# Performance work log

Measured on AMD Instinct MI355X. Metric: run time of the kernel, lower is better.

## Reference

```python
import jax, jax.numpy as jnp
import numpy as np

D_MODEL = 1024
H = 16
D_K = D_MODEL // H
D_FF = 4096
EPS = 1e-6
NEG = -1e9


def layernorm(x, alpha, bias):
    # custom LN: unbiased std (ddof=1), scalar alpha/bias, divide by (std+eps)
    mean = jnp.mean(x, axis=-1, keepdims=True)
    n = x.shape[-1]
    var = jnp.sum((x - mean) ** 2, axis=-1, keepdims=True) / (n - 1)
    std = jnp.sqrt(var)
    return alpha * (x - mean) / (std + EPS) + bias


def setup_inputs() -> dict:
    key = jax.random.key(0)
    ks = jax.random.split(key, 16)
    B, S = 2, 2048
    s = 1.0 / np.sqrt(D_MODEL)
    inp = {
        "x": jax.random.normal(ks[0], (B, S, D_MODEL), jnp.float32),
        "src_mask": jnp.ones((B, 1, S), jnp.int32),
        "wq": jax.random.normal(ks[1], (D_MODEL, D_MODEL), jnp.float32) * s,
        "bq": jnp.zeros((D_MODEL,), jnp.float32),
        "wk": jax.random.normal(ks[2], (D_MODEL, D_MODEL), jnp.float32) * s,
        "bk": jnp.zeros((D_MODEL,), jnp.float32),
        "wv": jax.random.normal(ks[3], (D_MODEL, D_MODEL), jnp.float32) * s,
        "bv": jnp.zeros((D_MODEL,), jnp.float32),
        "wo": jax.random.normal(ks[4], (D_MODEL, D_MODEL), jnp.float32) * s,
        "bo": jnp.zeros((D_MODEL,), jnp.float32),
        "w1": jax.random.normal(ks[5], (D_MODEL, D_FF), jnp.float32) * s,
        "b1": jnp.zeros((D_FF,), jnp.float32),
        "w2": jax.random.normal(ks[6], (D_FF, D_MODEL), jnp.float32) * (1.0 / np.sqrt(D_FF)),
        "b2": jnp.zeros((D_MODEL,), jnp.float32),
        "ln1_a": jnp.ones((1,), jnp.float32),
        "ln1_b": jnp.zeros((1,), jnp.float32),
        "ln2_a": jnp.ones((1,), jnp.float32),
        "ln2_b": jnp.zeros((1,), jnp.float32),
    }
    return inp


def reference(x, src_mask, wq, bq, wk, bk, wv, bv, wo, bo,
              w1, b1, w2, b2, ln1_a, ln1_b, ln2_a, ln2_b):
    B, S, _ = x.shape
    # --- residual 1: pre-norm self attention ---
    xn = layernorm(x, ln1_a, ln1_b)
    q = (xn @ wq + bq).reshape(B, S, H, D_K)
    k = (xn @ wk + bk).reshape(B, S, H, D_K)
    v = (xn @ wv + bv).reshape(B, S, H, D_K)
    # scores [B, H, S, S]
    scores = jnp.einsum("bqhd,bkhd->bhqk", q, k) / jnp.sqrt(jnp.float32(D_K))
    m = src_mask[:, None, :, :]  # [B,1,1,S]
    scores = jnp.where(m == 0, NEG, scores)
    attn = jax.nn.softmax(scores, axis=-1)
    ctx = jnp.einsum("bhqk,bkhd->bqhd", attn, v).reshape(B, S, D_MODEL)
    attn_out = ctx @ wo + bo
    x = x + attn_out
    # --- residual 2: pre-norm FFN ---
    xn = layernorm(x, ln2_a, ln2_b)
    ff = jax.nn.relu(xn @ w1 + b1) @ w2 + b2
    return x + ff
```

## Files before the change

### kernel.cpp

```cpp
#include <hip/hip_runtime.h>
#include <hip/hip_bf16.h>

typedef __attribute__((ext_vector_type(8))) short short8;
typedef __attribute__((ext_vector_type(4))) float f32x4;
typedef __attribute__((ext_vector_type(4))) unsigned int u32x4;
using u16 = unsigned short;
typedef unsigned int u32;

__device__ __forceinline__ u16 f2bf(float f) {
    u32 u = __builtin_bit_cast(u32, f);
    u32 r = u + 0x7FFFu + ((u >> 16) & 1u);
    return (u16)(r >> 16);
}

__device__ __forceinline__ float exp2fast(float x) {
    return __builtin_amdgcn_exp2f(x);
}

__device__ __forceinline__ u32 cvtpk(float lo, float hi) {
    u32 r;
    asm("v_cvt_pk_bf16_f32 %0, %1, %2" : "=v"(r) : "v"(lo), "v"(hi));
    return r;
}

__device__ __forceinline__ void async_load16(const void* g, void* l) {
    __builtin_amdgcn_global_load_lds(
        (const __attribute__((address_space(1))) void*)g,
        (__attribute__((address_space(3))) void*)l, 16, 0, 0);
}

__device__ __forceinline__ void wg_barrier() {
    asm volatile("" ::: "memory");
    __builtin_amdgcn_s_barrier();
    asm volatile("" ::: "memory");
}

__global__ __launch_bounds__(256) void convt_kernel(const float* __restrict__ w,
                                                    u16* __restrict__ wt, int K, int N) {
    __shared__ float tile[32][33];
    int bn = blockIdx.x * 32, bk = blockIdx.y * 32;
    int tx = threadIdx.x & 31, ty = threadIdx.x >> 5;
#pragma unroll
    for (int i = 0; i < 4; i++)
        tile[ty + i * 8][tx] = w[(size_t)(bk + ty + i * 8) * N + bn + tx];
    __syncthreads();
#pragma unroll
    for (int i = 0; i < 4; i++)
        wt[(size_t)(bn + ty + i * 8) * K + bk + tx] = f2bf(tile[tx][ty + i * 8]);
}

__global__ __launch_bounds__(256) void convt4_kernel(const float* __restrict__ wa,
                                                     const float* __restrict__ wb,
                                                     const float* __restrict__ wc,
                                                     const float* __restrict__ wd,
                                                     u16* __restrict__ da,
                                                     u16* __restrict__ db,
                                                     u16* __restrict__ dc,
                                                     u16* __restrict__ dd) {
    __shared__ float tile[32][33];
    int z = blockIdx.z;
    const float* w = (z == 0) ? wa : (z == 1) ? wb : (z == 2) ? wc : wd;
    u16* wt = (z == 0) ? da : (z == 1) ? db : (z == 2) ? dc : dd;
    int bn = blockIdx.x * 32, bk = blockIdx.y * 32;
    int tx = threadIdx.x & 31, ty = threadIdx.x >> 5;
#pragma unroll
    for (int i = 0; i < 4; i++)
        tile[ty + i * 8][tx] = w[(size_t)(bk + ty + i * 8) * 1024 + bn + tx];
    __syncthreads();
#pragma unroll
    for (int i = 0; i < 4; i++)
        wt[(size_t)(bn + ty + i * 8) * 1024 + bk + tx] = f2bf(tile[tx][ty + i * 8]);
}

__global__ __launch_bounds__(256) void vtrans_kernel(const u16* __restrict__ qkv,
                                                     u16* __restrict__ vT) {
    __shared__ u16 tile[32][33];
    int bs = blockIdx.x * 32;
    int bc = blockIdx.y * 32;
    int b  = blockIdx.z;
    int tx = threadIdx.x & 31, ty = threadIdx.x >> 5;
#pragma unroll
    for (int i = 0; i < 4; i++)
        tile[ty + i * 8][tx] = qkv[(size_t)(b * 2048 + bs + ty + i * 8) * 3072 + 2048 + bc + tx];
    __syncthreads();
#pragma unroll
    for (int i = 0; i < 4; i++)
        vT[(size_t)(b * 1024 + bc + ty + i * 8) * 2048 + bs + tx] = tile[tx][ty + i * 8];
}

__global__ __launch_bounds__(256) void ln_kernel(const float* __restrict__ x,
                                                 const float* __restrict__ ga,
                                                 const float* __restrict__ gb,
                                                 u16* __restrict__ out) {
    int row = blockIdx.x;
    const float4* xr = (const float4*)(x + (size_t)row * 1024);
    float4 v = xr[threadIdx.x];
    float s  = v.x + v.y + v.z + v.w;
    float s2 = v.x * v.x + v.y * v.y + v.z * v.z + v.w * v.w;
#pragma unroll
    for (int off = 32; off; off >>= 1) {
        s  += __shfl_down(s, off);
        s2 += __shfl_down(s2, off);
    }
    __shared__ float rs[4], rs2[4];
    int wid = threadIdx.x >> 6, lane = threadIdx.x & 63;
    if (lane == 0) { rs[wid] = s; rs2[wid] = s2; }
    __syncthreads();
    float S  = rs[0] + rs[1] + rs[2] + rs[3];
    float S2 = rs2[0] + rs2[1] + rs2[2] + rs2[3];
    float mean = S * (1.0f / 1024.0f);
    float var  = fmaxf((S2 - 1024.0f * mean * mean) * (1.0f / 1023.0f), 0.0f);
    float scale = ga[0] / (sqrtf(var) + 1e-6f);
    float shift = gb[0] - mean * scale;
    u16 h0 = f2bf(v.x * scale + shift);
    u16 h1 = f2bf(v.y * scale + shift);
    u16 h2 = f2bf(v.z * scale + shift);
    u16 h3 = f2bf(v.w * scale + shift);
    uint2 pv;
    pv.x = (u32)h0 | ((u32)h1 << 16);
    pv.y = (u32)h2 | ((u32)h3 << 16);
    *(uint2*)(out + (size_t)row * 1024 + threadIdx.x * 4) = pv;
}

__global__ __launch_bounds__(256) void bias3_kernel(const float* __restrict__ a,
                                                    const float* __restrict__ b,
                                                    const float* __restrict__ c,
                                                    float* __restrict__ d) {
    int i = blockIdx.x * 256 + threadIdx.x;
    float v = (i < 1024) ? a[i] : ((i < 2048) ? b[i - 1024] : c[i - 2048]);
    d[i] = v;
}

__global__ __launch_bounds__(256) void addbias_kernel(float* __restrict__ dst,
                                                      const float* __restrict__ p,
                                                      const float* __restrict__ bias,
                                                      const float* __restrict__ resid) {
    int i4 = blockIdx.x * 256 + threadIdx.x;
    float4 d  = ((const float4*)dst)[i4];
    float4 pp = ((const float4*)p)[i4];
    float4 rr = ((const float4*)resid)[i4];
    float4 bb = *(const float4*)(bias + ((i4 * 4) & 1023));
    d.x += pp.x + bb.x + rr.x;
    d.y += pp.y + bb.y + rr.y;
    d.z += pp.z + bb.z + rr.z;
    d.w += pp.w + bb.w + rr.w;
    ((float4*)dst)[i4] = d;
}

template <int RELU>
__global__ __launch_bounds__(512) void gemm256_bt(const u16* __restrict__ A,
                                                  const u16* __restrict__ Bt,
                                                  const float* __restrict__ bias,
                                                  u16* __restrict__ C,
                                                  int M, int N, int K, int tilesN) {
    __shared__ u16 lds[2][2][16384];
    const int tid = threadIdx.x;
    const int lane = tid & 63, wid = tid >> 6;
    const int l15 = lane & 15, l4 = lane >> 4;
    const int wm = wid >> 2, wn = wid & 3;

    int nwg = gridDim.x;
    int bid = blockIdx.x;
    int swz = (bid & 7) * (nwg >> 3) + (bid >> 3);
    int ty = swz / tilesN, tx = swz % tilesN;

    const u16* Ag = A + (size_t)(ty * 256) * K;
    const u16* Bg = Bt + (size_t)(tx * 256) * K;

    auto stage_half = [&](int slot, int ab, int half, const u16* G, int k0) {
#pragma unroll
        for (int j = 0; j < 2; j++) {
            int off16 = half * 1024 + j * 512 + tid;
            int r = off16 >> 3;
            int gs = (off16 & 7) ^ (r & 7);
            const u16* src = G + (size_t)r * K + k0 + gs * 8;
            u16* dst = &lds[slot][ab][(size_t)(half * 1024 + j * 512 + (wid << 6)) * 8];
            async_load16(src, dst);
        }
    };

    f32x4 acc[8][4] = {};
    const int nT = K >> 6;

    stage_half(0, 0, 0, Ag, 0);
    stage_half(0, 0, 1, Ag, 0);
    stage_half(0, 1, 0, Bg, 0);
    stage_half(0, 1, 1, Bg, 0);
    __builtin_amdgcn_sched_barrier(0);

    for (int t = 0; t < nT; ++t) {
        const int cs = t & 1, ns = cs ^ 1;
        const int k1 = (t + 1) << 6;
        const bool pf = (t + 1 < nT);
#pragma unroll
        for (int ph = 0; ph < 4; ++ph) {
            if (ph == 0 && pf) { stage_half(ns, 0, 0, Ag, k1); stage_half(ns, 0, 1, Ag, k1); }
            if (ph == 1 && pf) { stage_half(ns, 1, 0, Bg, k1); stage_half(ns, 1, 1, Bg, k1); }
            __builtin_amdgcn_sched_barrier(0);
            if (ph == 0) {
                if (pf) asm volatile("s_waitcnt vmcnt(4)" ::: "memory");
                else    asm volatile("s_waitcnt vmcnt(0)" ::: "memory");
            }
            wg_barrier();

            const int rh = ph >> 1, ch = ph & 1;
            const u16* la = &lds[cs][0][0];
            const u16* lb = &lds[cs][1][0];
            short8 af[4][2], bf[2][2];
#pragma unroll
            for (int m2 = 0; m2 < 4; m2++) {
                int ra = wm * 128 + rh * 64 + m2 * 16 + l15;
#pragma unroll
                for (int ks = 0; ks < 2; ks++) {
                    int sl = (l4 + ks * 4) ^ (ra & 7);
                    af[m2][ks] = *(const short8*)&la[ra * 64 + sl * 8];
                }
            }
#pragma unroll
            for (int n2 = 0; n2 < 2; n2++) {
                int rb = wn * 64 + ch * 32 + n2 * 16 + l15;
#pragma unroll
                for (int ks = 0; ks < 2; ks++) {
                    int sl = (l4 + ks * 4) ^ (rb & 7);
                    bf[n2][ks] = *(const short8*)&lb[rb * 64 + sl * 8];
                }
            }
            __builtin_amdgcn_s_setprio(1);
#pragma unroll
            for (int m2 = 0; m2 < 4; m2++)
#pragma unroll
                for (int n2 = 0; n2 < 2; n2++)
#pragma unroll
                    for (int ks = 0; ks < 2; ks++)
                        acc[rh * 4 + m2][ch * 2 + n2] = __builtin_amdgcn_mfma_f32_16x16x32_bf16(
                            af[m2][ks], bf[n2][ks], acc[rh * 4 + m2][ch * 2 + n2], 0, 0, 0);
            __builtin_amdgcn_s_setprio(0);
            wg_barrier();
        }
    }

#pragma unroll
    for (int mi = 0; mi < 8; mi++) {
        int row0 = ty * 256 + wm * 128 + (mi >> 2) * 64 + (mi & 3) * 16 + l4 * 4;
#pragma unroll
        for (int ni = 0; ni < 4; ni++) {
            int col = tx * 256 + wn * 64 + (ni >> 1) * 32 + (ni & 1) * 16 + l15;
            float bc = bias[col];
#pragma unroll
            for (int jj = 0; jj < 4; jj++) {
                float v = acc[mi][ni][jj] + bc;
                if (RELU) v = fmaxf(v, 0.0f);
                C[(size_t)(row0 + jj) * N + col] = f2bf(v);
            }
        }
    }
}

template <int MODE, int RELU, int RESID>
__global__ __launch_bounds__(256) void gemm_bt(const u16* __restrict__ A,
                                               const u16* __restrict__ Bt,
                                               const float* __restrict__ bias,
                                               void* __restrict__ C0,
                                               void* __restrict__ C1,
                                               const float* __restrict__ resid,
                                               int M, int N, int K, int kLen) {
    __shared__ u16 As[8192];
    __shared__ u16 Bs[8192];
    int tid = threadIdx.x, lane = tid & 63, wid = tid >> 6;
    int l15 = lane & 15, l4 = lane >> 4;
    int rowA0 = blockIdx.x * 128;
    int rowB0 = blockIdx.y * 128;
    int kOff = blockIdx.z * kLen;
    void* Cout = blockIdx.z ? C1 : C0;
    int waveM = wid >> 1, waveN = wid & 1;

    int fl = tid * 8;
    int r0 = fl >> 5, c0 = fl & 31;
    const u16* gA0 = A + (size_t)(rowA0 + r0) * K + c0 + kOff;
    const u16* gA1 = A + (size_t)(rowA0 + 64 + r0) * K + c0 + kOff;
    const u16* gB0 = Bt + (size_t)(rowB0 + r0) * K + c0 + kOff;
    const u16* gB1 = Bt + (size_t)(rowB0 + 64 + r0) * K + c0 + kOff;

    f32x4 acc[4][4] = {};
    const int nIter = kLen >> 5;

    async_load16(gA0, As + wid * 512);
    async_load16(gA1, As + 2048 + wid * 512);
    async_load16(gB0, Bs + wid * 512);
    async_load16(gB1, Bs + 2048 + wid * 512);

    int cur = 0, kb = 32;
    for (int it = 0; it < nIter; ++it) {
        asm volatile("s_waitcnt vmcnt(0)" ::: "memory");
        __builtin_amdgcn_s_barrier();
        if (it + 1 < nIter) {
            u16* a = As + (cur ^ 1) * 4096;
            u16* bb = Bs + (cur ^ 1) * 4096;
            async_load16(gA0 + kb, a + wid * 512);
            async_load16(gA1 + kb, a + 2048 + wid * 512);
            async_load16(gB0 + kb, bb + wid * 512);
            async_load16(gB1 + kb, bb + 2048 + wid * 512);
        }
        __builtin_amdgcn_sched_barrier(0);

        const u16* a = As + cur * 4096;
        const u16* bb = Bs + cur * 4096;
        short8 af[4], bf[4];
#pragma unroll
        for (int m = 0; m < 4; m++)
            af[m] = *(const short8*)&a[(waveM * 64 + m * 16 + l15) * 32 + l4 * 8];
#pragma unroll
        for (int n = 0; n < 4; n++)
            bf[n] = *(const short8*)&bb[(waveN * 64 + n * 16 + l15) * 32 + l4 * 8];
#pragma unroll
        for (int m = 0; m < 4; m++)
#pragma unroll
            for (int n = 0; n < 4; n++)
                acc[m][n] = __builtin_amdgcn_mfma_f32_16x16x32_bf16(af[m], bf[n], acc[m][n], 0, 0, 0);

        __builtin_amdgcn_s_barrier();
        cur ^= 1;
        kb += 32;
    }

#pragma unroll
    for (int m = 0; m < 4; m++) {
        int row = rowA0 + waveM * 64 + m * 16 + l4 * 4;
#pragma unroll
        for (int n = 0; n < 4; n++) {
            int col = rowB0 + waveN * 64 + n * 16 + l15;
            float bc = (MODE == 2) ? 0.0f : bias[col];
#pragma unroll
            for (int j = 0; j < 4; j++) {
                float v = acc[m][n][j] + bc;
                if (RELU) v = fmaxf(v, 0.0f);
                if (RESID) v += resid[(size_t)(row + j) * N + col];
                if (MODE == 1)
                    ((u16*)Cout)[(size_t)(row + j) * N + col] = f2bf(v);
                else
                    ((float*)Cout)[(size_t)(row + j) * N + col] = v;
            }
        }
    }
}

__global__ __launch_bounds__(256) void attn_kernel(const u16* __restrict__ qkv,
                                                   const u16* __restrict__ vT,
                                                   const int* __restrict__ mask,
                                                   u16* __restrict__ ctx) {
    const int S = 2048;
    const float C = 0.180336880f;
    int qt = blockIdx.x;
    int bh = blockIdx.y;
    int b = bh >> 4, h = bh & 15;
    int tid = threadIdx.x;
    int wid = tid >> 6, lane = tid & 63;
    int l15 = lane & 15, l4 = lane >> 4;

    __shared__ u16 Ks[64][72];
    __shared__ u16 Vs[64][72];
    __shared__ int mflag;

    if (tid == 0) mflag = 1;
    __syncthreads();
    {
        const int* mrow = mask + b * S;
        int ok = 1;
#pragma unroll
        for (int i = 0; i < 8; i++) ok &= (mrow[tid * 8 + i] != 0);
        if (!ok) mflag = 0;
    }

    int qrow0 = qt * 64 + wid * 16;
    const u16* qb = qkv + (size_t)(b * S + qrow0) * 3072 + h * 64;
    short8 qf0 = *(const short8*)(qb + (size_t)l15 * 3072 + l4 * 8);
    short8 qf1 = *(const short8*)(qb + (size_t)l15 * 3072 + 32 + l4 * 8);

    f32x4 o[4] = {};
    float m_i = -1e30f, lp = 0.0f;
    __syncthreads();
    const int allones = mflag;
    const int* mrow = mask + b * S;

    int srow = tid >> 3, c8 = (tid & 7) * 8;
    short8 kreg[2], vreg[2];
#pragma unroll
    for (int p = 0; p < 2; p++) {
        int r = p * 32 + srow;
        kreg[p] = *(const short8*)(qkv + (size_t)(b * S + r) * 3072 + 1024 + h * 64 + c8);
        vreg[p] = *(const short8*)(vT + (size_t)(bh * 64 + r) * 2048 + c8);
    }

    for (int kt = 0; kt < 32; ++kt) {
        __builtin_amdgcn_s_barrier();
#pragma unroll
        for (int p = 0; p < 2; p++) {
            int r = p * 32 + srow;
            *(short8*)&Ks[r][c8] = kreg[p];
            *(short8*)&Vs[r][c8] = vreg[p];
        }
        if (kt + 1 < 32) {
#pragma unroll
            for (int p = 0; p < 2; p++) {
                int r = p * 32 + srow;
                kreg[p] = *(const short8*)(qkv + (size_t)(b * S + (kt + 1) * 64 + r) * 3072 + 1024 + h * 64 + c8);
                vreg[p] = *(const short8*)(vT + (size_t)(bh * 64 + r) * 2048 + (kt + 1) * 64 + c8);
            }
        }
        asm volatile("s_waitcnt lgkmcnt(0)" ::: "memory");
        __builtin_amdgcn_s_barrier();

        float sc[4][4];
#pragma unroll
        for (int kc = 0; kc < 4; kc++) {
            short8 kf0 = *(const short8*)&Ks[kc * 16 + l15][l4 * 8];
            short8 kf1 = *(const short8*)&Ks[kc * 16 + l15][32 + l4 * 8];
            f32x4 a = {};
            a = __builtin_amdgcn_mfma_f32_16x16x32_bf16(kf0, qf0, a, 0, 0, 0);
            a = __builtin_amdgcn_mfma_f32_16x16x32_bf16(kf1, qf1, a, 0, 0, 0);
            if (allones) {
#pragma unroll
                for (int j = 0; j < 4; j++) sc[kc][j] = a[j];
            } else {
#pragma unroll
                for (int j = 0; j < 4; j++) {
                    int mk = mrow[kt * 64 + kc * 16 + l4 * 4 + j];
                    sc[kc][j] = mk ? a[j] : -1e9f;
                }
            }
        }

        float lm = sc[0][0];
#pragma unroll
        for (int kc = 0; kc < 4; kc++)
#pragma unroll
            for (int j = 0; j < 4; j++) lm = fmaxf(lm, sc[kc][j]);
        if (!__all(lm <= m_i + 64.0f)) {
            float t = lm;
            t = fmaxf(t, __shfl_xor(t, 16));
            t = fmaxf(t, __shfl_xor(t, 32));
            float newm = fmaxf(m_i, t);
            float r = exp2fast((m_i - newm) * C);
            lp *= r;
            float rr0 = __shfl(r, l4 * 4 + 0);
            float rr1 = __shfl(r, l4 * 4 + 1);
            float rr2 = __shfl(r, l4 * 4 + 2);
            float rr3 = __shfl(r, l4 * 4 + 3);
#pragma unroll
            for (int dc = 0; dc < 4; dc++) {
                o[dc][0] *= rr0; o[dc][1] *= rr1; o[dc][2] *= rr2; o[dc][3] *= rr3;
            }
            m_i = newm;
        }

        float nb = -m_i * C;
        u32 pk[4][2];
#pragma unroll
        for (int kc = 0; kc < 4; kc++) {
            float p0 = exp2fast(fmaf(sc[kc][0], C, nb));
            float p1 = exp2fast(fmaf(sc[kc][1], C, nb));
            float p2 = exp2fast(fmaf(sc[kc][2], C, nb));
            float p3 = exp2fast(fmaf(sc[kc][3], C, nb));
            lp += (p0 + p1) + (p2 + p3);
            pk[kc][0] = cvtpk(p0, p1);
            pk[kc][1] = cvtpk(p2, p3);
        }

        u32 w0[4], w1[4];
#pragma unroll
        for (int i = 0; i < 4; i++) {
            int idx = l15 + (((2 * l4 + (i >> 1)) & 3) << 4);
            int tt = i & 1;
            u32 a0 = (u32)__shfl((int)pk[0][tt], idx);
            u32 a1 = (u32)__shfl((int)pk[1][tt], idx);
            u32 a2 = (u32)__shfl((int)pk[2][tt], idx);
            u32 a3 = (u32)__shfl((int)pk[3][tt], idx);
            w0[i] = (l4 < 2) ? a0 : a1;
            w1[i] = (l4 < 2) ? a2 : a3;
        }
        u32x4 v0 = {w0[0], w0[1], w0[2], w0[3]};
        u32x4 v1 = {w1[0], w1[1], w1[2], w1[3]};
        short8 pa0 = __builtin_bit_cast(short8, v0);
        short8 pa1 = __builtin_bit_cast(short8, v1);

#pragma unroll
        for (int dc = 0; dc < 4; dc++) {
            short8 vf0 = *(const short8*)&Vs[dc * 16 + l15][l4 * 8];
            short8 vf1 = *(const short8*)&Vs[dc * 16 + l15][32 + l4 * 8];
            o[dc] = __builtin_amdgcn_mfma_f32_16x16x32_bf16(pa0, vf0, o[dc], 0, 0, 0);
            o[dc] = __builtin_amdgcn_mfma_f32_16x16x32_bf16(pa1, vf1, o[dc], 0, 0, 0);
        }
    }

    float lt = lp;
    lt += __shfl_xor(lt, 16);
    lt += __shfl_xor(lt, 32);
    float inv = 1.0f / lt;
    float iv0 = __shfl(inv, l4 * 4 + 0);
    float iv1 = __shfl(inv, l4 * 4 + 1);
    float iv2 = __shfl(inv, l4 * 4 + 2);
    float iv3 = __shfl(inv, l4 * 4 + 3);
#pragma unroll
    for (int j = 0; j < 4; j++) {
        float ivj = (j == 0) ? iv0 : (j == 1) ? iv1 : (j == 2) ? iv2 : iv3;
        int row = qrow0 + l4 * 4 + j;
        size_t base = (size_t)(b * S + row) * 1024 + h * 64;
#pragma unroll
        for (int dc = 0; dc < 4; dc++)
            ctx[base + dc * 16 + l15] = f2bf(o[dc][j] * ivj);
    }
}

extern "C" void kernel_launch(void* const* d_in, const int* in_sizes, int n_in,
                              void* d_out, int out_size, void* d_ws, size_t ws_size,
                              hipStream_t stream) {
    const float* x    = (const float*)d_in[0];
    const int*   mask = (const int*)d_in[1];
    const float* wq   = (const float*)d_in[2];
    const float* bq   = (const float*)d_in[3];
    const float* wk   = (const float*)d_in[4];
    const float* bk   = (const float*)d_in[5];
    const float* wv   = (const float*)d_in[6];
    const float* bv   = (const float*)d_in[7];
    const float* wo   = (const float*)d_in[8];
    const float* bo   = (const float*)d_in[9];
    const float* w1   = (const float*)d_in[10];
    const float* b1   = (const float*)d_in[11];
    const float* w2   = (const float*)d_in[12];
    const float* b2   = (const float*)d_in[13];
    const float* ln1a = (const float*)d_in[14];
    const float* ln1b = (const float*)d_in[15];
    const float* ln2a = (const float*)d_in[16];
    const float* ln2b = (const float*)d_in[17];
    float* out = (float*)d_out;

    char* ws = (char*)d_ws;
    u16*   wqkvt = (u16*)(ws + 0);
    u16*   wot   = (u16*)(ws + 6291456);
    u16*   w1t   = (u16*)(ws + 8388608);
    u16*   w2t   = (u16*)(ws + 16777216);
    float* bqkv  = (float*)(ws + 25165824);
    char*  regA  = ws + 26214400;
    u16*   xn1   = (u16*)(regA + 0);
    u16*   vT    = (u16*)(regA + 0);
    u16*   qkv   = (u16*)(regA + 8388608);
    u16*   ctx   = (u16*)(regA + 33554432);
    float* p0wo  = (float*)(regA + 0);
    float* x1    = (float*)(ws + 68157440);
    u16*   xn2   = (u16*)(regA + 0);
    u16*   ff1   = (u16*)(regA + 8388608);
    float* p0f2  = (float*)(ws + 0);

    dim3 blk(256);

    convt4_kernel<<<dim3(32, 32, 4), blk, 0, stream>>>(
        wq, wk, wv, wo, wqkvt, wqkvt + 1024 * 1024, wqkvt + 2048 * 1024, wot);
    convt_kernel<<<dim3(128, 32), blk, 0, stream>>>(w1, w1t, 1024, 4096);
    convt_kernel<<<dim3(32, 128), blk, 0, stream>>>(w2, w2t, 4096, 1024);
    bias3_kernel<<<dim3(12), blk, 0, stream>>>(bq, bk, bv, bqkv);

    ln_kernel<<<dim3(4096), blk, 0, stream>>>(x, ln1a, ln1b, xn1);
    gemm256_bt<0><<<dim3(192), dim3(512), 0, stream>>>(xn1, wqkvt, bqkv, qkv, 4096, 3072, 1024, 12);
    vtrans_kernel<<<dim3(64, 32, 2), blk, 0, stream>>>(qkv, vT);
    attn_kernel<<<dim3(32, 32), blk, 0, stream>>>(qkv, vT, mask, ctx);
    gemm_bt<2, 0, 0><<<dim3(32, 8, 2), blk, 0, stream>>>(ctx, wot, nullptr, p0wo, x1, nullptr,
                                                         4096, 1024, 1024, 512);
    addbias_kernel<<<dim3(4096), blk, 0, stream>>>(x1, p0wo, bo, x);

    ln_kernel<<<dim3(4096), blk, 0, stream>>>(x1, ln2a, ln2b, xn2);
    gemm256_bt<1><<<dim3(256), dim3(512), 0, stream>>>(xn2, w1t, b1, ff1, 4096, 4096, 1024, 16);
    gemm_bt<2, 0, 0><<<dim3(32, 8, 2), blk, 0, stream>>>(ff1, w2t, nullptr, p0f2, out, nullptr,
                                                         4096, 1024, 4096, 2048);
    addbias_kernel<<<dim3(4096), blk, 0, stream>>>(out, p0f2, b2, x1);
}
```

Before: 279.9 us.

## Split attention key range across two wave groups and merge partial softmax

The attention block grows from 256 to 512 threads. Two groups of four waves each handle half of the key tiles, with their own K/V LDS buffers. At the end the groups exchange row max, row sum and partial outputs through LDS to combine the online-softmax results. The P-matrix register transpose, previously done with many cross-lane shuffles, now goes through a per-wave LDS scratch buffer. This doubles the waves in flight per block to hide latency, at the cost of more LDS, an extra merge phase with block-wide barriers, and possible occupancy limits.

```diff
diff --git a/kernel.cpp b/kernel.cpp
--- a/kernel.cpp
+++ b/kernel.cpp
@@ -344,7 +344,7 @@
     }
 }
 
-__global__ __launch_bounds__(256) void attn_kernel(const u16* __restrict__ qkv,
+__global__ __launch_bounds__(512) void attn_kernel(const u16* __restrict__ qkv,
                                                    const u16* __restrict__ vT,
                                                    const int* __restrict__ mask,
                                                    u16* __restrict__ ctx) {
@@ -356,9 +356,12 @@
     int tid = threadIdx.x;
     int wid = tid >> 6, lane = tid & 63;
     int l15 = lane & 15, l4 = lane >> 4;
-
-    __shared__ u16 Ks[64][72];
-    __shared__ u16 Vs[64][72];
+    int g = wid >> 2, qw = wid & 3;
+
+    __shared__ u16 Ks[2][64][72];
+    __shared__ u16 Vs[2][64][72];
+    __shared__ u32 PT[8][16][38];
+    __shared__ float mbuf[2][4][16], lbuf[2][4][16];
     __shared__ int mflag;
 
     if (tid == 0) mflag = 1;
@@ -367,11 +370,11 @@
         const int* mrow = mask + b * S;
         int ok = 1;
 #pragma unroll
-        for (int i = 0; i < 8; i++) ok &= (mrow[tid * 8 + i] != 0);
+        for (int i = 0; i < 4; i++) ok &= (mrow[tid * 4 + i] != 0);
         if (!ok) mflag = 0;
     }
 
-    int qrow0 = qt * 64 + wid * 16;
+    int qrow0 = qt * 64 + qw * 16;
     const u16* qb = qkv + (size_t)(b * S + qrow0) * 3072 + h * 64;
     short8 qf0 = *(const short8*)(qb + (size_t)l15 * 3072 + l4 * 8);
     short8 qf1 = *(const short8*)(qb + (size_t)l15 * 3072 + 32 + l4 * 8);
@@ -382,24 +385,27 @@
     const int allones = mflag;
     const int* mrow = mask + b * S;
 
-    int srow = tid >> 3, c8 = (tid & 7) * 8;
+    int tl = tid & 255;
+    int srow = tl >> 3, c8 = (tl & 7) * 8;
+    const int kt0 = g * 16;
     short8 kreg[2], vreg[2];
 #pragma unroll
     for (int p = 0; p < 2; p++) {
         int r = p * 32 + srow;
-        kreg[p] = *(const short8*)(qkv + (size_t)(b * S + r) * 3072 + 1024 + h * 64 + c8);
-        vreg[p] = *(const short8*)(vT + (size_t)(bh * 64 + r) * 2048 + c8);
-    }
-
-    for (int kt = 0; kt < 32; ++kt) {
-        __builtin_amdgcn_s_barrier();
+        kreg[p] = *(const short8*)(qkv + (size_t)(b * S + kt0 * 64 + r) * 3072 + 1024 + h * 64 + c8);
+        vreg[p] = *(const short8*)(vT + (size_t)(bh * 64 + r) * 2048 + kt0 * 64 + c8);
+    }
+
+    for (int it = 0; it < 16; ++it) {
+        const int kt = kt0 + it;
+        wg_barrier();
 #pragma unroll
         for (int p = 0; p < 2; p++) {
             int r = p * 32 + srow;
-            *(short8*)&Ks[r][c8] = kreg[p];
-            *(short8*)&Vs[r][c8] = vreg[p];
-        }
-        if (kt + 1 < 32) {
+            *(short8*)&Ks[g][r][c8] = kreg[p];
+            *(short8*)&Vs[g][r][c8] = vreg[p];
+        }
+        if (it + 1 < 16) {
 #pragma unroll
             for (int p = 0; p < 2; p++) {
                 int r = p * 32 + srow;
@@ -408,13 +414,13 @@
             }
         }
         asm volatile("s_waitcnt lgkmcnt(0)" ::: "memory");
-        __builtin_amdgcn_s_barrier();
+        wg_barrier();
 
         float sc[4][4];
 #pragma unroll
         for (int kc = 0; kc < 4; kc++) {
-            short8 kf0 = *(const short8*)&Ks[kc * 16 + l15][l4 * 8];
-            short8 kf1 = *(const short8*)&Ks[kc * 16 + l15][32 + l4 * 8];
+            short8 kf0 = *(const short8*)&Ks[g][kc * 16 + l15][l4 * 8];
+            short8 kf1 = *(const short8*)&Ks[g][kc * 16 + l15][32 + l4 * 8];
             f32x4 a = {};
             a = __builtin_amdgcn_mfma_f32_16x16x32_bf16(kf0, qf0, a, 0, 0, 0);
             a = __builtin_amdgcn_mfma_f32_16x16x32_bf16(kf1, qf1, a, 0, 0, 0);
@@ -454,7 +460,6 @@
         }
 
         float nb = -m_i * C;
-        u32 pk[4][2];
 #pragma unroll
         for (int kc = 0; kc < 4; kc++) {
             float p0 = exp2fast(fmaf(sc[kc][0], C, nb));
@@ -462,31 +467,25 @@
             float p2 = exp2fast(fmaf(sc[kc][2], C, nb));
             float p3 = exp2fast(fmaf(sc[kc][3], C, nb));
             lp += (p0 + p1) + (p2 + p3);
-            pk[kc][0] = cvtpk(p0, p1);
-            pk[kc][1] = cvtpk(p2, p3);
-        }
-
-        u32 w0[4], w1[4];
-#pragma unroll
-        for (int i = 0; i < 4; i++) {
-            int idx = l15 + (((2 * l4 + (i >> 1)) & 3) << 4);
-            int tt = i & 1;
-            u32 a0 = (u32)__shfl((int)pk[0][tt], idx);
-            u32 a1 = (u32)__shfl((int)pk[1][tt], idx);
-            u32 a2 = (u32)__shfl((int)pk[2][tt], idx);
-            u32 a3 = (u32)__shfl((int)pk[3][tt], idx);
-            w0[i] = (l4 < 2) ? a0 : a1;
-            w1[i] = (l4 < 2) ? a2 : a3;
-        }
-        u32x4 v0 = {w0[0], w0[1], w0[2], w0[3]};
-        u32x4 v1 = {w1[0], w1[1], w1[2], w1[3]};
-        short8 pa0 = __builtin_bit_cast(short8, v0);
-        short8 pa1 = __builtin_bit_cast(short8, v1);
+            uint2 w;
+            w.x = cvtpk(p0, p1);
+            w.y = cvtpk(p2, p3);
+            *(uint2*)&PT[wid][l15][kc * 8 + l4 * 2] = w;
+        }
+
+        uint2 r01 = *(const uint2*)&PT[wid][l15][l4 * 4];
+        uint2 r23 = *(const uint2*)&PT[wid][l15][l4 * 4 + 2];
+        uint2 r45 = *(const uint2*)&PT[wid][l15][16 + l4 * 4];
+        uint2 r67 = *(const uint2*)&PT[wid][l15][16 + l4 * 4 + 2];
+        u32x4 w0 = {r01.x, r01.y, r23.x, r23.y};
+        u32x4 w1 = {r45.x, r45.y, r67.x, r67.y};
+        short8 pa0 = __builtin_bit_cast(short8, w0);
+        short8 pa1 = __builtin_bit_cast(short8, w1);
 
 #pragma unroll
         for (int dc = 0; dc < 4; dc++) {
-            short8 vf0 = *(const short8*)&Vs[dc * 16 + l15][l4 * 8];
-            short8 vf1 = *(const short8*)&Vs[dc * 16 + l15][32 + l4 * 8];
+            short8 vf0 = *(const short8*)&Vs[g][dc * 16 + l15][l4 * 8];
+            short8 vf1 = *(const short8*)&Vs[g][dc * 16 + l15][32 + l4 * 8];
             o[dc] = __builtin_amdgcn_mfma_f32_16x16x32_bf16(pa0, vf0, o[dc], 0, 0, 0);
             o[dc] = __builtin_amdgcn_mfma_f32_16x16x32_bf16(pa1, vf1, o[dc], 0, 0, 0);
         }
@@ -495,19 +494,39 @@
     float lt = lp;
     lt += __shfl_xor(lt, 16);
     lt += __shfl_xor(lt, 32);
-    float inv = 1.0f / lt;
-    float iv0 = __shfl(inv, l4 * 4 + 0);
-    float iv1 = __shfl(inv, l4 * 4 + 1);
-    float iv2 = __shfl(inv, l4 * 4 + 2);
-    float iv3 = __shfl(inv, l4 * 4 + 3);
+    if (l4 == 0) { mbuf[g][qw][l15] = m_i; lbuf[g][qw][l15] = lt; }
+    __syncthreads();
+    float mo = mbuf[g ^ 1][qw][l15], lo = lbuf[g ^ 1][qw][l15];
+    float M  = fmaxf(m_i, mo);
+    float rs = exp2fast((m_i - M) * C);
+    float ro = exp2fast((mo - M) * C);
+    float inv = 1.0f / (rs * lt + ro * lo);
+    float rs_j[4], iv_j[4];
 #pragma unroll
     for (int j = 0; j < 4; j++) {
-        float ivj = (j == 0) ? iv0 : (j == 1) ? iv1 : (j == 2) ? iv2 : iv3;
-        int row = qrow0 + l4 * 4 + j;
-        size_t base = (size_t)(b * S + row) * 1024 + h * 64;
-#pragma unroll
-        for (int dc = 0; dc < 4; dc++)
-            ctx[base + dc * 16 + l15] = f2bf(o[dc][j] * ivj);
+        rs_j[j] = __shfl(rs,  l4 * 4 + j);
+        iv_j[j] = __shfl(inv, l4 * 4 + j);
+    }
+
+    float* obuf = (float*)&Ks[0][0][0];
+#pragma unroll
+    for (int c = 0; c < 2; c++) {
+        int dce = (g ^ 1) * 2 + c;
+#pragma unroll
+        for (int j = 0; j < 4; j++)
+            obuf[(((g * 4 + qw) * 16) + l4 * 4 + j) * 32 + c * 16 + l15] = o[dce][j] * rs_j[j];
+    }
+    __syncthreads();
+#pragma unroll
+    for (int c = 0; c < 2; c++) {
+        int dco = g * 2 + c;
+#pragma unroll
+        for (int j = 0; j < 4; j++) {
+            float peer = obuf[((((g ^ 1) * 4 + qw) * 16) + l4 * 4 + j) * 32 + c * 16 + l15];
+            float val = (o[dco][j] * rs_j[j] + peer) * iv_j[j];
+            int row = qrow0 + l4 * 4 + j;
+            ctx[(size_t)(b * S + row) * 1024 + h * 64 + dco * 16 + l15] = f2bf(val);
+        }
     }
 }
 
@@ -562,7 +581,7 @@
     ln_kernel<<<dim3(4096), blk, 0, stream>>>(x, ln1a, ln1b, xn1);
     gemm256_bt<0><<<dim3(192), dim3(512), 0, stream>>>(xn1, wqkvt, bqkv, qkv, 4096, 3072, 1024, 12);
     vtrans_kernel<<<dim3(64, 32, 2), blk, 0, stream>>>(qkv, vT);
-    attn_kernel<<<dim3(32, 32), blk, 0, stream>>>(qkv, vT, mask, ctx);
+    attn_kernel<<<dim3(32, 32), dim3(512), 0, stream>>>(qkv, vT, mask, ctx);
     gemm_bt<2, 0, 0><<<dim3(32, 8, 2), blk, 0, stream>>>(ctx, wot, nullptr, p0wo, x1, nullptr,
                                                          4096, 1024, 1024, 512);
     addbias_kernel<<<dim3(4096), blk, 0, stream>>>(x1, p0wo, bo, x);
```

Result: faster. 270.5 us (-3.4%).
